# Optimization experiments

Measured on AMD Instinct MI355X. Metric: run time of the kernel, lower is better.

Reference implementation:

```python
import jax, jax.numpy as jnp
import numpy as np

N_NODES = 100000
N_EDGES = 3200000


def setup_inputs() -> dict:
    key = jax.random.key(0)
    ks = jax.random.split(key, 16)
    inp = {
        "noisy_coords": jax.random.normal(ks[0], (N_NODES, 3), dtype=jnp.float32),
        "atom_types": jax.random.randint(ks[1], (N_NODES,), 0, 2),
        "edge_index": jax.random.randint(ks[2], (2, N_EDGES), 0, N_NODES),
        "emb": jax.random.normal(ks[3], (2, 3), dtype=jnp.float32),
    }
    # GCNConv weights: 6->32->64->64->32->3 (hidden_dim=64)
    dims = [(6, 32), (32, 64), (64, 64), (64, 32), (32, 3)]
    for i, (din, dout) in enumerate(dims, start=1):
        inp[f"W{i}"] = jax.random.normal(ks[3 + i], (din, dout), dtype=jnp.float32) / np.sqrt(din).astype(np.float32)
        inp[f"b{i}"] = jnp.zeros((dout,), dtype=jnp.float32)
    return inp


def _gcn_conv(x, W, b, src, dst, norm, n):
    # GCNConv: X @ W, then symmetric-normalized scatter-add over edges, then bias.
    h = x @ W                       # [N, dout]
    msg = h[src] * norm[:, None]    # gather + edge normalization  [E+N, dout]
    return jax.ops.segment_sum(msg, dst, num_segments=n) + b


def reference(noisy_coords, atom_types, edge_index, emb,
              W1, b1, W2, b2, W3, b3, W4, b4, W5, b5):
    n = noisy_coords.shape[0]
    loop = jnp.arange(n)
    # PyG GCNConv adds self loops and uses deg^{-1/2} (A+I) deg^{-1/2} normalization
    src = jnp.concatenate([edge_index[0], loop])
    dst = jnp.concatenate([edge_index[1], loop])
    deg = jax.ops.segment_sum(jnp.ones(src.shape[0], dtype=jnp.float32), dst, num_segments=n)
    dinv = jnp.where(deg > 0, jax.lax.rsqrt(deg), 0.0)
    norm = dinv[src] * dinv[dst]    # [E+N]

    x = jnp.concatenate([noisy_coords, emb[atom_types]], axis=1)  # [N, 6]
    x = jax.nn.relu(_gcn_conv(x, W1, b1, src, dst, norm, n))
    x = jax.nn.relu(_gcn_conv(x, W2, b2, src, dst, norm, n))
    x = jax.nn.relu(_gcn_conv(x, W3, b3, src, dst, norm, n))
    x = jax.nn.relu(_gcn_conv(x, W4, b4, src, dst, norm, n))
    x = _gcn_conv(x, W5, b5, src, dst, norm, n)  # final layer: no relu
    return x
```

## Files before the change

kernel.cpp:

```cpp
#include <hip/hip_runtime.h>
#include <hip/hip_fp16.h>

#define NBLK_BIN 256
#define NBKT 196
#define BWIN 512
#define CAP 128


typedef unsigned int uint;

union U32H2 { uint u; __half2 h; };

__device__ inline float2 h2_to_f2(uint u) {
    U32H2 c; c.u = u;
    return __half22float2(c.h);
}
__device__ inline uint f2_to_h2(float a, float b) {
    U32H2 c; c.h = __floats2half2_rn(a, b);
    return c.u;
}

__global__ __launch_bounds__(1024) void bin_kernel(const int* __restrict__ src,
                                                   const int* __restrict__ dst,
                                                   int2* __restrict__ pairs,
                                                   int* __restrict__ blkcnt, int e) {
    __shared__ int lcnt[NBKT];
    int blk = blockIdx.x, tid = threadIdx.x;
    for (int t = tid; t < NBKT; t += 1024) lcnt[t] = 0;
    __syncthreads();
    int chunk = (e + NBLK_BIN - 1) / NBLK_BIN;
    int base = blk * chunk;
    int end = min(e, base + chunk);
    for (int i = base + tid; i < end; i += 1024) {
        int s = src[i], d = dst[i];
        int b = d >> 9;
        int pos = atomicAdd(&lcnt[b], 1);
        if (pos < CAP) pairs[((size_t)blk * NBKT + b) * CAP + pos] = make_int2(s, d);
    }
    __syncthreads();
    for (int t = tid; t < NBKT; t += 1024) blkcnt[blk * NBKT + t] = min(lcnt[t], CAP);
}

__global__ __launch_bounds__(1024) void fill_kernel(const int2* __restrict__ pairs,
                                                    const int* __restrict__ blkcnt,
                                                    int* __restrict__ srcs,
                                                    int* __restrict__ cnt,
                                                    int* __restrict__ rowptr,
                                                    float* __restrict__ dinv, int n) {
    __shared__ int lc[BWIN];
    __shared__ int ps[BWIN];
    __shared__ int sm[NBLK_BIN];
    __shared__ int gbase_s;
    int b = blockIdx.x, tid = threadIdx.x;
    int nbase = b << 9;
    if (tid < BWIN) lc[tid] = 0;
    for (int t = tid; t < NBLK_BIN; t += 1024) sm[t] = blkcnt[t * NBKT + b];
    if (tid == 0) gbase_s = 0;
    __syncthreads();
    {
        long long tot = (long long)NBLK_BIN * b;
        int lsum = 0;
        for (long long j = tid; j < tot; j += 1024) {
            int blk = (int)(j / b);
            int bp  = (int)(j - (long long)blk * b);
            lsum += blkcnt[blk * NBKT + bp];
        }
        for (int o = 32; o > 0; o >>= 1) lsum += __shfl_down(lsum, o, 64);
        if ((tid & 63) == 0 && lsum != 0) atomicAdd(&gbase_s, lsum);
    }
    int wave = tid >> 6, lane = tid & 63;
    for (int blk = wave; blk < NBLK_BIN; blk += 16) {
        int m = sm[blk];
        const int2* p = pairs + ((size_t)blk * NBKT + b) * CAP;
        for (int i = lane; i < m; i += 64) atomicAdd(&lc[p[i].y - nbase], 1);
    }
    __syncthreads();
    int myc = (tid < BWIN) ? lc[tid] : 0;
    if (tid < BWIN) ps[tid] = myc;
    __syncthreads();
    for (int off = 1; off < BWIN; off <<= 1) {
        int t = 0;
        if (tid < BWIN && tid >= off) t = ps[tid - off];
        __syncthreads();
        if (tid < BWIN) ps[tid] += t;
        __syncthreads();
    }
    int gbase = gbase_s;
    if (tid < BWIN) {
        int ex = ps[tid] - myc;
        int vtx = nbase + tid;
        if (vtx < n) {
            cnt[vtx] = myc;
            rowptr[vtx] = gbase + ex;
            dinv[vtx] = rsqrtf(1.0f + (float)myc);
        }
    }
    __syncthreads();
    if (tid < BWIN) lc[tid] = ps[tid] - myc;
    __syncthreads();
    for (int blk = wave; blk < NBLK_BIN; blk += 16) {
        int m = sm[blk];
        const int2* p = pairs + ((size_t)blk * NBKT + b) * CAP;
        for (int i = lane; i < m; i += 64) {
            int2 e2 = p[i];
            int o = atomicAdd(&lc[e2.y - nbase], 1);
            srcs[gbase + o] = e2.x;
        }
    }
}


__global__ __launch_bounds__(256) void build_x0_h_kernel(const float* __restrict__ coords,
                                                         const int* __restrict__ at,
                                                         const float* __restrict__ emb,
                                                         const float* __restrict__ dinv,
                                                         uint* __restrict__ x, int n) {
    int v = blockIdx.x * 256 + threadIdx.x;
    if (v >= n) return;
    float dv = dinv[v];
    float c0 = coords[3 * v + 0] * dv;
    float c1 = coords[3 * v + 1] * dv;
    float c2 = coords[3 * v + 2] * dv;
    int t = at[v];
    float e0 = emb[3 * t + 0] * dv;
    float e1 = emb[3 * t + 1] * dv;
    float e2 = emb[3 * t + 2] * dv;
    uint* row = x + (size_t)v * 4;
    row[0] = f2_to_h2(c0, c1);
    row[1] = f2_to_h2(c2, e0);
    row[2] = f2_to_h2(e1, e2);
    row[3] = 0;
}

template <int TPN, bool HAS_BIAS, bool RELU>
__global__ __launch_bounds__(256) void agg_v4_kernel(const uint* __restrict__ in_,
                                                     const float* __restrict__ dinv,
                                                     const int* __restrict__ rowptr,
                                                     const int* __restrict__ cnt,
                                                     const int* __restrict__ srcs,
                                                     const float* __restrict__ bias,
                                                     uint* __restrict__ out_, int n) {
    const uint4* in = (const uint4*)in_;
    uint4* out = (uint4*)out_;
    int gid = blockIdx.x * 256 + threadIdx.x;
    int v = gid / TPN, q = gid % TPN;
    if (v >= n) return;
    float ax[4], ay[4];
    {
        uint4 s0 = in[(size_t)v * TPN + q];
        uint su[4] = {s0.x, s0.y, s0.z, s0.w};
#pragma unroll
        for (int u = 0; u < 4; ++u) { float2 f = h2_to_f2(su[u]); ax[u] = f.x; ay[u] = f.y; }
    }
    int start = rowptr[v];
    int len = cnt[v];
    int k = 0;
    for (; k + 4 <= len; k += 4) {
        int sA = srcs[start + k];
        int sB = srcs[start + k + 1];
        int sC = srcs[start + k + 2];
        int sD = srcs[start + k + 3];
        uint4 fA = in[(size_t)sA * TPN + q];
        uint4 fB = in[(size_t)sB * TPN + q];
        uint4 fC = in[(size_t)sC * TPN + q];
        uint4 fD = in[(size_t)sD * TPN + q];
        uint ua[4] = {fA.x, fA.y, fA.z, fA.w};
        uint ub[4] = {fB.x, fB.y, fB.z, fB.w};
        uint uc[4] = {fC.x, fC.y, fC.z, fC.w};
        uint ud[4] = {fD.x, fD.y, fD.z, fD.w};
#pragma unroll
        for (int u = 0; u < 4; ++u) {
            float2 a = h2_to_f2(ua[u]);
            float2 b = h2_to_f2(ub[u]);
            float2 c = h2_to_f2(uc[u]);
            float2 d = h2_to_f2(ud[u]);
            ax[u] += (a.x + b.x) + (c.x + d.x);
            ay[u] += (a.y + b.y) + (c.y + d.y);
        }
    }
    for (; k < len; ++k) {
        int s = srcs[start + k];
        uint4 f = in[(size_t)s * TPN + q];
        uint uu[4] = {f.x, f.y, f.z, f.w};
#pragma unroll
        for (int u = 0; u < 4; ++u) { float2 t = h2_to_f2(uu[u]); ax[u] += t.x; ay[u] += t.y; }
    }
    float dv = dinv[v];
#pragma unroll
    for (int u = 0; u < 4; ++u) {
        ax[u] *= dv; ay[u] *= dv;
        if (HAS_BIAS) { ax[u] += bias[8 * q + 2 * u]; ay[u] += bias[8 * q + 2 * u + 1]; }
        if (RELU) { ax[u] = fmaxf(ax[u], 0.0f); ay[u] = fmaxf(ay[u], 0.0f); }
    }
    uint4 o;
    o.x = f2_to_h2(ax[0], ay[0]);
    o.y = f2_to_h2(ax[1], ay[1]);
    o.z = f2_to_h2(ax[2], ay[2]);
    o.w = f2_to_h2(ax[3], ay[3]);
    out[(size_t)v * TPN + q] = o;
}

__global__ __launch_bounds__(256) void agg_l4l5_kernel(const uint* __restrict__ in_,
                                                       const float* __restrict__ dinv,
                                                       const int* __restrict__ rowptr,
                                                       const int* __restrict__ cnt,
                                                       const int* __restrict__ srcs,
                                                       const float* __restrict__ b4,
                                                       const float* __restrict__ W5,
                                                       float* __restrict__ outf, int n) {
    const uint4* in = (const uint4*)in_;
    int gid = blockIdx.x * 256 + threadIdx.x;
    int v = gid >> 2, q = gid & 3;
    if (v >= n) return;
    float ax[4], ay[4];
    {
        uint4 s0 = in[(size_t)v * 4 + q];
        uint su[4] = {s0.x, s0.y, s0.z, s0.w};
#pragma unroll
        for (int u = 0; u < 4; ++u) { float2 f = h2_to_f2(su[u]); ax[u] = f.x; ay[u] = f.y; }
    }
    int start = rowptr[v];
    int len = cnt[v];
    int k = 0;
    for (; k + 4 <= len; k += 4) {
        int sA = srcs[start + k];
        int sB = srcs[start + k + 1];
        int sC = srcs[start + k + 2];
        int sD = srcs[start + k + 3];
        uint4 fA = in[(size_t)sA * 4 + q];
        uint4 fB = in[(size_t)sB * 4 + q];
        uint4 fC = in[(size_t)sC * 4 + q];
        uint4 fD = in[(size_t)sD * 4 + q];
        uint ua[4] = {fA.x, fA.y, fA.z, fA.w};
        uint ub[4] = {fB.x, fB.y, fB.z, fB.w};
        uint uc[4] = {fC.x, fC.y, fC.z, fC.w};
        uint ud[4] = {fD.x, fD.y, fD.z, fD.w};
#pragma unroll
        for (int u = 0; u < 4; ++u) {
            float2 a = h2_to_f2(ua[u]);
            float2 b = h2_to_f2(ub[u]);
            float2 c = h2_to_f2(uc[u]);
            float2 d = h2_to_f2(ud[u]);
            ax[u] += (a.x + b.x) + (c.x + d.x);
            ay[u] += (a.y + b.y) + (c.y + d.y);
        }
    }
    for (; k < len; ++k) {
        int s = srcs[start + k];
        uint4 f = in[(size_t)s * 4 + q];
        uint uu[4] = {f.x, f.y, f.z, f.w};
#pragma unroll
        for (int u = 0; u < 4; ++u) { float2 t = h2_to_f2(uu[u]); ax[u] += t.x; ay[u] += t.y; }
    }
    float dv = dinv[v];
    float feat[8];
#pragma unroll
    for (int u = 0; u < 4; ++u) {
        float fx = ax[u] * dv + b4[8 * q + 2 * u];
        float fy = ay[u] * dv + b4[8 * q + 2 * u + 1];
        feat[2 * u]     = fmaxf(fx, 0.0f);
        feat[2 * u + 1] = fmaxf(fy, 0.0f);
    }
    float p0 = 0.f, p1 = 0.f, p2 = 0.f;
#pragma unroll
    for (int m = 0; m < 8; ++m) {
        int j = 8 * q + m;
        p0 = fmaf(feat[m], W5[j * 3 + 0], p0);
        p1 = fmaf(feat[m], W5[j * 3 + 1], p1);
        p2 = fmaf(feat[m], W5[j * 3 + 2], p2);
    }
#pragma unroll
    for (int m = 1; m < 4; m <<= 1) {
        p0 += __shfl_xor(p0, m, 4);
        p1 += __shfl_xor(p1, m, 4);
        p2 += __shfl_xor(p2, m, 4);
    }
    float o = (q == 0) ? p0 : (q == 1 ? p1 : (q == 2 ? p2 : 0.0f));
    outf[(size_t)v * 4 + q] = (q < 3) ? o * dv : 0.0f;
}

template <int DIN, int DOUT, int DOUTH2, bool HAS_BIAS, bool RELU, bool SCALE>
__global__ __launch_bounds__(256) void gemm_h_kernel(const uint* __restrict__ xin,
                                                     const float* __restrict__ W,
                                                     const float* __restrict__ bias,
                                                     const float* __restrict__ dinv,
                                                     uint* __restrict__ xout,
                                                     int istride_u, int ostride, int n) {
    __shared__ float wlds[DIN * DOUT];
    for (int i = threadIdx.x; i < DIN * DOUT; i += 256) wlds[i] = W[i];
    __syncthreads();
    int gid = blockIdx.x * 256 + threadIdx.x;
    int v = gid / DOUTH2, j2 = gid % DOUTH2;
    if (v >= n) return;
    int j1 = 2 * j2;
    const uint* xr = xin + (size_t)v * istride_u;
    float acc0 = 0.0f, acc1 = 0.0f;
#pragma unroll
    for (int ku = 0; ku < DIN / 2; ++ku) {
        float2 xf = h2_to_f2(xr[ku]);
        int k = 2 * ku;
        acc0 = fmaf(xf.x, wlds[k * DOUT + j1], acc0);
        acc0 = fmaf(xf.y, wlds[(k + 1) * DOUT + j1], acc0);
        if (j1 + 1 < DOUT) {
            acc1 = fmaf(xf.x, wlds[k * DOUT + j1 + 1], acc1);
            acc1 = fmaf(xf.y, wlds[(k + 1) * DOUT + j1 + 1], acc1);
        }
    }
    if (HAS_BIAS) {
        acc0 += bias[j1];
        if (j1 + 1 < DOUT) acc1 += bias[j1 + 1];
    }
    if (RELU) { acc0 = fmaxf(acc0, 0.0f); acc1 = fmaxf(acc1, 0.0f); }
    if (SCALE) { float dv = dinv[v]; acc0 *= dv; acc1 *= dv; }
    xout[(size_t)v * ostride + j2] = f2_to_h2(acc0, acc1);
}

#define G34_NODES 16
__global__ __launch_bounds__(256) void gemm34_kernel(const uint* __restrict__ xin,
                                                     const float* __restrict__ W3,
                                                     const float* __restrict__ b3,
                                                     const float* __restrict__ W4,
                                                     const float* __restrict__ dinv,
                                                     uint* __restrict__ xout,
                                                     int n) {
    __shared__ float4 w3c[16][64];
    __shared__ float4 w4c[16][32];
    __shared__ float4 hb4[16][17];
    for (int idx = threadIdx.x; idx < 16 * 64; idx += 256) {
        int kc = idx >> 6, c = idx & 63;
        w3c[kc][c] = make_float4(W3[(4 * kc + 0) * 64 + c], W3[(4 * kc + 1) * 64 + c],
                                 W3[(4 * kc + 2) * 64 + c], W3[(4 * kc + 3) * 64 + c]);
    }
    for (int idx = threadIdx.x; idx < 16 * 32; idx += 256) {
        int kc = idx >> 5, c = idx & 31;
        w4c[kc][c] = make_float4(W4[(4 * kc + 0) * 32 + c], W4[(4 * kc + 1) * 32 + c],
                                 W4[(4 * kc + 2) * 32 + c], W4[(4 * kc + 3) * 32 + c]);
    }
    __syncthreads();
    int i  = threadIdx.x >> 4;
    int j2 = threadIdx.x & 15;
    int v  = blockIdx.x * G34_NODES + i;
    bool ok = (v < n);

    float acc[4] = {0.f, 0.f, 0.f, 0.f};
    if (ok) {
        const uint4* xr = (const uint4*)(xin + (size_t)v * 32);
        for (int kb = 0; kb < 8; ++kb) {
            uint4 xa = xr[kb];
            float2 f0 = h2_to_f2(xa.x);
            float2 f1 = h2_to_f2(xa.y);
            float2 f2v = h2_to_f2(xa.z);
            float2 f3 = h2_to_f2(xa.w);
            float xf0 = f0.x, xf1 = f0.y, xf2 = f1.x, xf3 = f1.y;
            float xf4 = f2v.x, xf5 = f2v.y, xf6 = f3.x, xf7 = f3.y;
#pragma unroll
            for (int u = 0; u < 4; ++u) {
                int c = j2 + 16 * u;
                float4 wa = w3c[2 * kb][c];
                float4 wb = w3c[2 * kb + 1][c];
                acc[u] = fmaf(xf0, wa.x, acc[u]);
                acc[u] = fmaf(xf1, wa.y, acc[u]);
                acc[u] = fmaf(xf2, wa.z, acc[u]);
                acc[u] = fmaf(xf3, wa.w, acc[u]);
                acc[u] = fmaf(xf4, wb.x, acc[u]);
                acc[u] = fmaf(xf5, wb.y, acc[u]);
                acc[u] = fmaf(xf6, wb.z, acc[u]);
                acc[u] = fmaf(xf7, wb.w, acc[u]);
            }
        }
    }
#pragma unroll
    for (int u = 0; u < 4; ++u) {
        int c = j2 + 16 * u;
        float h = ok ? fmaxf(acc[u] + b3[c], 0.0f) : 0.0f;
        ((float*)hb4)[i * 68 + c] = h;
    }
    __syncthreads();

    float a0 = 0.f, a1 = 0.f;
#pragma unroll
    for (int kc = 0; kc < 16; ++kc) {
        float4 h4  = hb4[i][kc];
        float4 wlo = w4c[kc][j2];
        float4 whi = w4c[kc][j2 + 16];
        a0 = fmaf(h4.x, wlo.x, a0);
        a0 = fmaf(h4.y, wlo.y, a0);
        a0 = fmaf(h4.z, wlo.z, a0);
        a0 = fmaf(h4.w, wlo.w, a0);
        a1 = fmaf(h4.x, whi.x, a1);
        a1 = fmaf(h4.y, whi.y, a1);
        a1 = fmaf(h4.z, whi.z, a1);
        a1 = fmaf(h4.w, whi.w, a1);
    }
    if (ok) {
        float dv = dinv[v];
        __half* o = (__half*)(xout + (size_t)v * 16);
        o[j2]      = __float2half(a0 * dv);
        o[j2 + 16] = __float2half(a1 * dv);
    }
}

__global__ __launch_bounds__(256) void agg_f4_kernel(const float* __restrict__ in_,
                                                     const float* __restrict__ dinv,
                                                     const int* __restrict__ rowptr,
                                                     const int* __restrict__ cnt,
                                                     const int* __restrict__ srcs,
                                                     const float* __restrict__ b,
                                                     float* __restrict__ out, int n) {
    const float4* in = (const float4*)in_;
    int v = blockIdx.x * 256 + threadIdx.x;
    if (v >= n) return;
    float4 s = in[v];
    float a0 = s.x, a1 = s.y, a2 = s.z;
    int start = rowptr[v];
    int len = cnt[v];
    int k = 0;
    for (; k + 4 <= len; k += 4) {
        int sA = srcs[start + k];
        int sB = srcs[start + k + 1];
        int sC = srcs[start + k + 2];
        int sD = srcs[start + k + 3];
        float4 fA = in[sA];
        float4 fB = in[sB];
        float4 fC = in[sC];
        float4 fD = in[sD];
        a0 += (fA.x + fB.x) + (fC.x + fD.x);
        a1 += (fA.y + fB.y) + (fC.y + fD.y);
        a2 += (fA.z + fB.z) + (fC.z + fD.z);
    }
    for (; k < len; ++k) {
        float4 f = in[srcs[start + k]];
        a0 += f.x; a1 += f.y; a2 += f.z;
    }
    float dv = dinv[v];
    out[(size_t)v * 3 + 0] = a0 * dv + b[0];
    out[(size_t)v * 3 + 1] = a1 * dv + b[1];
    out[(size_t)v * 3 + 2] = a2 * dv + b[2];
}


extern "C" void kernel_launch(void* const* d_in, const int* in_sizes, int n_in,
                              void* d_out, int out_size, void* d_ws, size_t ws_size,
                              hipStream_t stream) {
    const float* coords = (const float*)d_in[0];
    const int* at       = (const int*)d_in[1];
    const int* ei       = (const int*)d_in[2];
    const float* emb    = (const float*)d_in[3];
    const float* W1 = (const float*)d_in[4];  const float* b1 = (const float*)d_in[5];
    const float* W2 = (const float*)d_in[6];  const float* b2 = (const float*)d_in[7];
    const float* W3 = (const float*)d_in[8];  const float* b3 = (const float*)d_in[9];
    const float* W4 = (const float*)d_in[10]; const float* b4 = (const float*)d_in[11];
    const float* W5 = (const float*)d_in[12]; const float* b5 = (const float*)d_in[13];
    float* out = (float*)d_out;

    const int n = in_sizes[0] / 3;
    const int e = in_sizes[2] / 2;
    const int* src = ei;
    const int* dst = ei + e;

    char* ws = (char*)d_ws;
    size_t off = 0;
    float* dinv   = (float*)(ws + off); off += (size_t)n * 4;
    int*   cnt    = (int*)(ws + off);   off += (size_t)n * 4;
    int*   rowptr = (int*)(ws + off);   off += (size_t)n * 4;
    int*   blkcnt = (int*)(ws + off);   off += (size_t)NBLK_BIN * NBKT * 4;
    int*   srcs   = (int*)(ws + off);   off += (size_t)e * 4;
    char*  alias  = ws + off;
    int2*  pairs  = (int2*)alias;
    uint*  A_h    = (uint*)alias;
    uint*  B_h    = A_h + (size_t)n * 32;
    float* B_f    = (float*)(B_h + (size_t)n * 32);

    int nb = (n + 255) / 256;

    bin_kernel<<<NBLK_BIN, 1024, 0, stream>>>(src, dst, pairs, blkcnt, e);
    fill_kernel<<<NBKT, 1024, 0, stream>>>(pairs, blkcnt, srcs, cnt, rowptr, dinv, n);

    build_x0_h_kernel<<<nb, 256, 0, stream>>>(coords, at, emb, dinv, A_h, n);

    auto blocks = [](long long threads) { return (int)((threads + 255) / 256); };

    agg_v4_kernel<1, false, false><<<blocks((long long)n), 256, 0, stream>>>(
        A_h, dinv, rowptr, cnt, srcs, nullptr, B_h, n);
    gemm_h_kernel<6, 32, 16, true, true, true><<<blocks((long long)n * 16), 256, 0, stream>>>(
        B_h, W1, b1, dinv, A_h, 4, 16, n);

    agg_v4_kernel<4, false, false><<<blocks((long long)n * 4), 256, 0, stream>>>(
        A_h, dinv, rowptr, cnt, srcs, nullptr, B_h, n);
    gemm_h_kernel<32, 64, 32, true, true, true><<<blocks((long long)n * 32), 256, 0, stream>>>(
        B_h, W2, b2, dinv, A_h, 16, 32, n);

    agg_v4_kernel<8, false, false><<<blocks((long long)n * 8), 256, 0, stream>>>(
        A_h, dinv, rowptr, cnt, srcs, nullptr, B_h, n);
    gemm34_kernel<<<(n + G34_NODES - 1) / G34_NODES, 256, 0, stream>>>(
        B_h, W3, b3, W4, dinv, A_h, n);

    agg_l4l5_kernel<<<blocks((long long)n * 4), 256, 0, stream>>>(
        A_h, dinv, rowptr, cnt, srcs, b4, W5, B_f, n);

    agg_f4_kernel<<<blocks((long long)n), 256, 0, stream>>>(
        B_f, dinv, rowptr, cnt, srcs, b5, out, n);
}
```

Before: 412.7 us.

## Store hidden features in planar 16-byte slabs so aggregation blocks gather one slab

Node features switch from interleaved rows (node-major, all 16-byte chunks together) to a planar layout where each 16-byte chunk index forms its own contiguous slab of n entries. Aggregation blocks now each handle one slab for 256 nodes, so the random gathers of a block stay within a smaller array, meant to improve L2/MALL locality. The GEMM kernels are updated to read and write the new layout, which adds strided, less coalesced accesses there. The agg_l4l5 kernel keeps four threads per node but each now reads from a different slab.

```diff
diff --git a/kernel.cpp b/kernel.cpp
--- a/kernel.cpp
+++ b/kernel.cpp
@@ -133,21 +133,21 @@
 }
 
 template <int TPN, bool HAS_BIAS, bool RELU>
-__global__ __launch_bounds__(256) void agg_v4_kernel(const uint* __restrict__ in_,
-                                                     const float* __restrict__ dinv,
-                                                     const int* __restrict__ rowptr,
-                                                     const int* __restrict__ cnt,
-                                                     const int* __restrict__ srcs,
-                                                     const float* __restrict__ bias,
-                                                     uint* __restrict__ out_, int n) {
-    const uint4* in = (const uint4*)in_;
-    uint4* out = (uint4*)out_;
-    int gid = blockIdx.x * 256 + threadIdx.x;
-    int v = gid / TPN, q = gid % TPN;
+__global__ __launch_bounds__(256) void agg_v4p_kernel(const uint* __restrict__ in_,
+                                                      const float* __restrict__ dinv,
+                                                      const int* __restrict__ rowptr,
+                                                      const int* __restrict__ cnt,
+                                                      const int* __restrict__ srcs,
+                                                      const float* __restrict__ bias,
+                                                      uint* __restrict__ out_, int n) {
+    int q = blockIdx.x % TPN;
+    int v = (blockIdx.x / TPN) * 256 + threadIdx.x;
     if (v >= n) return;
+    const uint4* in = (const uint4*)in_ + (size_t)q * n;
+    uint4* out = (uint4*)out_ + (size_t)q * n;
     float ax[4], ay[4];
     {
-        uint4 s0 = in[(size_t)v * TPN + q];
+        uint4 s0 = in[v];
         uint su[4] = {s0.x, s0.y, s0.z, s0.w};
 #pragma unroll
         for (int u = 0; u < 4; ++u) { float2 f = h2_to_f2(su[u]); ax[u] = f.x; ay[u] = f.y; }
@@ -160,10 +160,10 @@
         int sB = srcs[start + k + 1];
         int sC = srcs[start + k + 2];
         int sD = srcs[start + k + 3];
-        uint4 fA = in[(size_t)sA * TPN + q];
-        uint4 fB = in[(size_t)sB * TPN + q];
-        uint4 fC = in[(size_t)sC * TPN + q];
-        uint4 fD = in[(size_t)sD * TPN + q];
+        uint4 fA = in[sA];
+        uint4 fB = in[sB];
+        uint4 fC = in[sC];
+        uint4 fD = in[sD];
         uint ua[4] = {fA.x, fA.y, fA.z, fA.w};
         uint ub[4] = {fB.x, fB.y, fB.z, fB.w};
         uint uc[4] = {fC.x, fC.y, fC.z, fC.w};
@@ -180,7 +180,7 @@
     }
     for (; k < len; ++k) {
         int s = srcs[start + k];
-        uint4 f = in[(size_t)s * TPN + q];
+        uint4 f = in[s];
         uint uu[4] = {f.x, f.y, f.z, f.w};
 #pragma unroll
         for (int u = 0; u < 4; ++u) { float2 t = h2_to_f2(uu[u]); ax[u] += t.x; ay[u] += t.y; }
@@ -197,7 +197,7 @@
     o.y = f2_to_h2(ax[1], ay[1]);
     o.z = f2_to_h2(ax[2], ay[2]);
     o.w = f2_to_h2(ax[3], ay[3]);
-    out[(size_t)v * TPN + q] = o;
+    out[v] = o;
 }
 
 __global__ __launch_bounds__(256) void agg_l4l5_kernel(const uint* __restrict__ in_,
@@ -208,13 +208,13 @@
                                                        const float* __restrict__ b4,
                                                        const float* __restrict__ W5,
                                                        float* __restrict__ outf, int n) {
-    const uint4* in = (const uint4*)in_;
     int gid = blockIdx.x * 256 + threadIdx.x;
     int v = gid >> 2, q = gid & 3;
     if (v >= n) return;
+    const uint4* in = (const uint4*)in_ + (size_t)q * n;
     float ax[4], ay[4];
     {
-        uint4 s0 = in[(size_t)v * 4 + q];
+        uint4 s0 = in[v];
         uint su[4] = {s0.x, s0.y, s0.z, s0.w};
 #pragma unroll
         for (int u = 0; u < 4; ++u) { float2 f = h2_to_f2(su[u]); ax[u] = f.x; ay[u] = f.y; }
@@ -227,10 +227,10 @@
         int sB = srcs[start + k + 1];
         int sC = srcs[start + k + 2];
         int sD = srcs[start + k + 3];
-        uint4 fA = in[(size_t)sA * 4 + q];
-        uint4 fB = in[(size_t)sB * 4 + q];
-        uint4 fC = in[(size_t)sC * 4 + q];
-        uint4 fD = in[(size_t)sD * 4 + q];
+        uint4 fA = in[sA];
+        uint4 fB = in[sB];
+        uint4 fC = in[sC];
+        uint4 fD = in[sD];
         uint ua[4] = {fA.x, fA.y, fA.z, fA.w};
         uint ub[4] = {fB.x, fB.y, fB.z, fB.w};
         uint uc[4] = {fC.x, fC.y, fC.z, fC.w};
@@ -247,7 +247,7 @@
     }
     for (; k < len; ++k) {
         int s = srcs[start + k];
-        uint4 f = in[(size_t)s * 4 + q];
+        uint4 f = in[s];
         uint uu[4] = {f.x, f.y, f.z, f.w};
 #pragma unroll
         for (int u = 0; u < 4; ++u) { float2 t = h2_to_f2(uu[u]); ax[u] += t.x; ay[u] += t.y; }
@@ -284,8 +284,7 @@
                                                      const float* __restrict__ W,
                                                      const float* __restrict__ bias,
                                                      const float* __restrict__ dinv,
-                                                     uint* __restrict__ xout,
-                                                     int istride_u, int ostride, int n) {
+                                                     uint* __restrict__ xout, int n) {
     __shared__ float wlds[DIN * DOUT];
     for (int i = threadIdx.x; i < DIN * DOUT; i += 256) wlds[i] = W[i];
     __syncthreads();
@@ -293,11 +292,10 @@
     int v = gid / DOUTH2, j2 = gid % DOUTH2;
     if (v >= n) return;
     int j1 = 2 * j2;
-    const uint* xr = xin + (size_t)v * istride_u;
     float acc0 = 0.0f, acc1 = 0.0f;
 #pragma unroll
     for (int ku = 0; ku < DIN / 2; ++ku) {
-        float2 xf = h2_to_f2(xr[ku]);
+        float2 xf = h2_to_f2(xin[(((size_t)(ku >> 2)) * n + v) * 4 + (ku & 3)]);
         int k = 2 * ku;
         acc0 = fmaf(xf.x, wlds[k * DOUT + j1], acc0);
         acc0 = fmaf(xf.y, wlds[(k + 1) * DOUT + j1], acc0);
@@ -312,7 +310,7 @@
     }
     if (RELU) { acc0 = fmaxf(acc0, 0.0f); acc1 = fmaxf(acc1, 0.0f); }
     if (SCALE) { float dv = dinv[v]; acc0 *= dv; acc1 *= dv; }
-    xout[(size_t)v * ostride + j2] = f2_to_h2(acc0, acc1);
+    xout[(((size_t)(j2 >> 2)) * n + v) * 4 + (j2 & 3)] = f2_to_h2(acc0, acc1);
 }
 
 #define G34_NODES 16
@@ -344,9 +342,9 @@
 
     float acc[4] = {0.f, 0.f, 0.f, 0.f};
     if (ok) {
-        const uint4* xr = (const uint4*)(xin + (size_t)v * 32);
+        const uint4* xp = (const uint4*)xin;
         for (int kb = 0; kb < 8; ++kb) {
-            uint4 xa = xr[kb];
+            uint4 xa = xp[(size_t)kb * n + v];
             float2 f0 = h2_to_f2(xa.x);
             float2 f1 = h2_to_f2(xa.y);
             float2 f2v = h2_to_f2(xa.z);
@@ -394,9 +392,10 @@
     }
     if (ok) {
         float dv = dinv[v];
-        __half* o = (__half*)(xout + (size_t)v * 16);
-        o[j2]      = __float2half(a0 * dv);
-        o[j2 + 16] = __float2half(a1 * dv);
+        __half* o = (__half*)xout;
+        int c0 = j2, c1 = j2 + 16;
+        o[((size_t)(c0 >> 3) * n + v) * 8 + (c0 & 7)] = __float2half(a0 * dv);
+        o[((size_t)(c1 >> 3) * n + v) * 8 + (c1 & 7)] = __float2half(a1 * dv);
     }
 }
 
@@ -480,17 +479,17 @@
 
     auto blocks = [](long long threads) { return (int)((threads + 255) / 256); };
 
-    agg_v4_kernel<1, false, false><<<blocks((long long)n), 256, 0, stream>>>(
+    agg_v4p_kernel<1, false, false><<<nb, 256, 0, stream>>>(
         A_h, dinv, rowptr, cnt, srcs, nullptr, B_h, n);
     gemm_h_kernel<6, 32, 16, true, true, true><<<blocks((long long)n * 16), 256, 0, stream>>>(
-        B_h, W1, b1, dinv, A_h, 4, 16, n);
-
-    agg_v4_kernel<4, false, false><<<blocks((long long)n * 4), 256, 0, stream>>>(
+        B_h, W1, b1, dinv, A_h, n);
+
+    agg_v4p_kernel<4, false, false><<<4 * nb, 256, 0, stream>>>(
         A_h, dinv, rowptr, cnt, srcs, nullptr, B_h, n);
     gemm_h_kernel<32, 64, 32, true, true, true><<<blocks((long long)n * 32), 256, 0, stream>>>(
-        B_h, W2, b2, dinv, A_h, 16, 32, n);
-
-    agg_v4_kernel<8, false, false><<<blocks((long long)n * 8), 256, 0, stream>>>(
+        B_h, W2, b2, dinv, A_h, n);
+
+    agg_v4p_kernel<8, false, false><<<8 * nb, 256, 0, stream>>>(
         A_h, dinv, rowptr, cnt, srcs, nullptr, B_h, n);
     gemm34_kernel<<<(n + G34_NODES - 1) / G34_NODES, 256, 0, stream>>>(
         B_h, W3, b3, W4, dinv, A_h, n);
@@ -498,6 +497,6 @@
     agg_l4l5_kernel<<<blocks((long long)n * 4), 256, 0, stream>>>(
         A_h, dinv, rowptr, cnt, srcs, b4, W5, B_f, n);
 
-    agg_f4_kernel<<<blocks((long long)n), 256, 0, stream>>>(
+    agg_f4_kernel<<<nb, 256, 0, stream>>>(
         B_f, dinv, rowptr, cnt, srcs, b5, out, n);
 }
```

New measurement: 622.0 us. +50.7%, slower.
